# Performance work log

Hardware: AMD Instinct MI355X
Metric: run time of the kernel (lower is better)

Reference implementation:

```python
import jax, jax.numpy as jnp
import numpy as np

B, T, F, H, K = 64, 256, 16, 128, 3


def setup_inputs() -> dict:
    key = jax.random.key(0)
    ks = jax.random.split(key, 8)
    s = 1.0 / np.sqrt(H)
    x = jax.random.normal(ks[0], (B, T, F), jnp.float32)
    index = jnp.sort(jax.random.randint(ks[1], (B, 2), 0, T), axis=1)
    # per-feature LSTM params (input dim 1), torch gate order [i, f, g, o]
    W_ih = jax.random.uniform(ks[2], (F, 4 * H), jnp.float32, -s, s)
    W_hh = jax.random.uniform(ks[3], (F, 4 * H, H), jnp.float32, -s, s)
    b = jax.random.uniform(ks[4], (F, 4 * H), jnp.float32, -s, s)  # b_ih + b_hh folded
    conv_w = jax.random.uniform(ks[5], (K,), jnp.float32, -1.0 / np.sqrt(K), 1.0 / np.sqrt(K))
    fc_w = jax.random.uniform(ks[6], (F * H, 2), jnp.float32, -1.0 / np.sqrt(F * H), 1.0 / np.sqrt(F * H))
    fc_b = jax.random.uniform(ks[7], (2,), jnp.float32, -1.0 / np.sqrt(F * H), 1.0 / np.sqrt(F * H))
    return dict(x=x, index=index, W_ih=W_ih, W_hh=W_hh, b=b, conv_w=conv_w, fc_w=fc_w, fc_b=fc_b)


def reference(x, index, W_ih, W_hh, b, conv_w, fc_w, fc_b):
    Bn, Tn, Fn = x.shape
    Hn = W_hh.shape[-1]
    t = jnp.arange(Tn)
    # valid[b, t] = start <= t < end; recurrence only advances inside the ragged slice
    valid = (t[None, :] >= index[:, 0:1]) & (t[None, :] < index[:, 1:2])  # [B, T]
    xs = jnp.moveaxis(x, 1, 0)            # [T, B, F]
    ms = jnp.moveaxis(valid, 1, 0)[:, :, None, None]  # [T, B, 1, 1]

    def step(carry, inp):
        h, c = carry                       # [B, F, H] each
        x_t, m = inp                       # [B, F], [B, 1, 1]
        gates = x_t[:, :, None] * W_ih[None] \
            + jnp.einsum('bfh,fgh->bfg', h, W_hh) + b[None]  # [B, F, 4H]
        i, f, g, o = jnp.split(gates, 4, axis=-1)
        i = jax.nn.sigmoid(i); f = jax.nn.sigmoid(f)
        g = jnp.tanh(g); o = jax.nn.sigmoid(o)
        c_new = f * c + i * g
        h_new = o * jnp.tanh(c_new)
        h = jnp.where(m, h_new, h)
        c = jnp.where(m, c_new, c)
        return (h, c), None

    h0 = jnp.zeros((Bn, Fn, Hn), x.dtype)
    (h, _), _ = jax.lax.scan(step, (h0, h0), (xs, ms))
    outs = h                               # [B, F, H] == last LSTM output per slice

    cofs = outs.mean(axis=-1)              # AdaptiveAvgPool1d(1) -> [B, F]
    cofs = jax.lax.conv_general_dilated(
        cofs[:, None, :], conv_w[None, None, :], (1,), [(K // 2, K // 2)],
        dimension_numbers=('NCH', 'OIH', 'NCH'))[:, 0, :]  # [B, F]
    gate = jax.nn.sigmoid(cofs)
    outs = outs * gate[:, :, None]
    return outs.reshape(Bn, -1) @ fc_w + fc_b  # [B, 2]
```

## Files before the change

### kernel.cpp

```cpp
#include <hip/hip_runtime.h>

typedef _Float16 half_t;
typedef half_t half2_t __attribute__((ext_vector_type(2)));
typedef half_t half8  __attribute__((ext_vector_type(8)));
typedef unsigned int uint_t;
typedef uint_t uint4v __attribute__((ext_vector_type(4)));
typedef float float4v __attribute__((ext_vector_type(4)));

#define B_  64
#define T_  256
#define F_  16
#define H_  128
#define LOG2E 1.44269504f

__device__ __forceinline__ float rcp_(float x)  { return __builtin_amdgcn_rcpf(x); }
__device__ __forceinline__ float sigm2(float x) { return rcp_(1.0f + __builtin_amdgcn_exp2f(x * -LOG2E)); }
__device__ __forceinline__ float tanh2(float x) { return fmaf(rcp_(1.0f + __builtin_amdgcn_exp2f(x * (-2.0f * LOG2E))), 2.0f, -1.0f); }
__device__ __forceinline__ float sigm(float x)  { return rcp_(1.0f + __expf(-x)); }

__global__ void make_sched(const int* __restrict__ index, int* __restrict__ pairs) {
    __shared__ int ss[B_], ee[B_], mid[B_], bo[B_];
    const int t = threadIdx.x;
    const int s = index[2 * t], e = index[2 * t + 1];
    ss[t] = s; ee[t] = e; mid[t] = s + e;
    __syncthreads();
    int m = mid[t], r = 0;
    for (int j = 0; j < B_; ++j) r += (mid[j] < m) || (mid[j] == m && j < t);
    bo[r] = t;
    __syncthreads();
    if (t < 32) {
        int bA = bo[2 * t], bB = bo[2 * t + 1];
        int su = min(ss[bA], ss[bB]), eu = max(ee[bA], ee[bB]);
        int4 v;
        v.x = (bA << 8) | bB;
        v.y = (ss[bA] << 16) | ee[bA];
        v.z = (ss[bB] << 16) | ee[bB];
        v.w = (su << 16) | eu;
        ((int4*)pairs)[t] = v;
    }
}

__global__ void repack_w(const float* __restrict__ whh, uint_t* __restrict__ wt) {
    const int f = blockIdx.x, w = blockIdx.y, tid = threadIdx.x;
    const int lane = tid & 63, q4 = tid >> 6;
    const int li = lane & 15, lg = lane >> 4;
    const float* base = whh + (size_t)f * 512 * 128;
#pragma unroll
    for (int qq = 0; qq < 4; ++qq) {
        const int qf = q4 * 4 + qq;
        const int m = qf >> 2, kt = qf & 3;
        const int g512 = 128 * m + 16 * w + li;
        uint_t tmp[4];
#pragma unroll
        for (int e2 = 0; e2 < 4; ++e2) {
            int k = kt * 32 + lg * 8 + 2 * e2;
            half2_t h;
            h[0] = (half_t)base[g512 * 128 + k];
            h[1] = (half_t)base[g512 * 128 + k + 1];
            tmp[e2] = __builtin_bit_cast(uint_t, h);
        }
        uint4 out = { tmp[0], tmp[1], tmp[2], tmp[3] };
        ((uint4*)wt)[(((size_t)f * 8 + w) * 16 + qf) * 64 + lane] = out;
    }
}

__global__ __launch_bounds__(512, 4) void lstm_mfma(
    const float* __restrict__ x, const uint_t* __restrict__ wt,
    const float* __restrict__ wih_g, const float* __restrict__ bias_g,
    const int* __restrict__ pairs, float* __restrict__ hout)
{
    __shared__ float xsh[2][T_];
    __shared__ alignas(16) half_t hbuf[2][2][H_];

    const int f = blockIdx.x & 15;
    const int4 pv = ((const int4*)pairs)[blockIdx.x >> 4];
    const int bA = pv.x >> 8, bB = pv.x & 255;
    const int sA = pv.y >> 16, eA = pv.y & 0xffff;
    const int sB = pv.z >> 16, eB = pv.z & 0xffff;
    const int su = pv.w >> 16, eu = pv.w & 0xffff;

    const int tid = threadIdx.x, lane = tid & 63, w = tid >> 6;
    const int li = lane & 15, lg = lane >> 4;
    const int cell = 16 * w + li;
    const int hsel = li >> 3;
    const int csel = lg >> 1;

    uint4v wr[16];
    {
        const char* ws = (const char*)wt + ((((size_t)f * 8 + w) * 16) * 64 + lane) * 16;
#pragma unroll
        for (int q = 0; q < 16; ++q) {
            unsigned long long a = (unsigned long long)(ws + (size_t)q * 1024);
            asm volatile("global_load_dwordx4 %0, %1, off" : "=v"(wr[q]) : "v"(a));
        }
        asm volatile("s_waitcnt vmcnt(0)");
        __builtin_amdgcn_sched_barrier(0);
    }

    float wih[4], bb4[4];
#pragma unroll
    for (int m = 0; m < 4; ++m) {
        wih[m] = wih_g[f * 512 + 128 * m + cell];
        bb4[m] = bias_g[f * 512 + 128 * m + cell];
    }

    const int myb = csel ? bB : bA;
    const int mys = csel ? sB : sA;
    const int mye = csel ? eB : eA;

    {
        int bb_ = tid >> 8, tt = tid & 255;
        xsh[bb_][tt] = x[((size_t)(bb_ ? bB : bA) * T_ + tt) * F_ + f];
    }
    if (tid < 2 * H_) hbuf[0][tid >> 7][tid & 127] = (half_t)0.0f;

    float cst = 0.0f, hst = 0.0f;
    int pp = 0;
    __syncthreads();

    for (int t = su; t < eu; ++t) {
        const half_t* hb = &hbuf[pp][hsel][lg * 8];
        half8 a0 = *(const half8*)(hb + 0);
        half8 a1 = *(const half8*)(hb + 32);
        half8 a2 = *(const half8*)(hb + 64);
        half8 a3 = *(const half8*)(hb + 96);
        float xt = xsh[csel][t];

        float gv[4];
#pragma unroll
        for (int m = 0; m < 4; ++m) {
            float iv = fmaf(xt, wih[m], bb4[m]);
            float4v ca = { iv, iv, iv, iv };
            float4v cb = { 0.f, 0.f, 0.f, 0.f };
            ca = __builtin_amdgcn_mfma_f32_16x16x32_f16(a0, __builtin_bit_cast(half8, wr[m * 4 + 0]), ca, 0, 0, 0);
            cb = __builtin_amdgcn_mfma_f32_16x16x32_f16(a1, __builtin_bit_cast(half8, wr[m * 4 + 1]), cb, 0, 0, 0);
            ca = __builtin_amdgcn_mfma_f32_16x16x32_f16(a2, __builtin_bit_cast(half8, wr[m * 4 + 2]), ca, 0, 0, 0);
            cb = __builtin_amdgcn_mfma_f32_16x16x32_f16(a3, __builtin_bit_cast(half8, wr[m * 4 + 3]), cb, 0, 0, 0);
            gv[m] = ca[0] + cb[0];
        }

        float gi = sigm2(gv[0]);
        float gf = sigm2(gv[1]);
        float gg = tanh2(gv[2]);
        float go = sigm2(gv[3]);
        float cn = fmaf(gf, cst, gi * gg);
        bool mk = (t >= mys) & (t < mye);
        cst = mk ? cn : cst;
        float hn = go * tanh2(cst);
        hst = mk ? hn : hst;

        if (lg == 0)      hbuf[pp ^ 1][0][cell] = (half_t)hst;
        else if (lg == 2) hbuf[pp ^ 1][1][cell] = (half_t)hst;
        __syncthreads();
        pp ^= 1;
    }

    if ((lg & 1) == 0) hout[((size_t)myb * F_ + f) * H_ + cell] = hst;
}

__global__ void epilogue(const float* __restrict__ hout, const float* __restrict__ conv_w,
                         const float* __restrict__ fc_w, const float* __restrict__ fc_b,
                         float* __restrict__ out)
{
    const int b = blockIdx.x, t = threadIdx.x;
    const int lane = t & 63, wv = t >> 6;
    __shared__ float part[2][16];
    __shared__ float gate_sh[16];

    float hv[16];
#pragma unroll
    for (int f = 0; f < 16; ++f) hv[f] = hout[((size_t)b * 16 + f) * 128 + t];

#pragma unroll
    for (int f = 0; f < 16; ++f) {
        float s = hv[f];
#pragma unroll
        for (int off = 32; off >= 1; off >>= 1) s += __shfl_down(s, off, 64);
        if (lane == 0) part[wv][f] = s;
    }
    __syncthreads();
    if (t < 16) gate_sh[t] = (part[0][t] + part[1][t]) * (1.0f / 128.0f);
    __syncthreads();
    float gate = 0.0f;
    if (t < 16) {
        float l  = (t > 0)  ? gate_sh[t - 1] : 0.0f;
        float mi = gate_sh[t];
        float r  = (t < 15) ? gate_sh[t + 1] : 0.0f;
        gate = sigm(fmaf(l, conv_w[0], fmaf(mi, conv_w[1], r * conv_w[2])));
    }
    __syncthreads();
    if (t < 16) gate_sh[t] = gate;
    __syncthreads();

    float acc0 = 0.0f, acc1 = 0.0f;
    const float2* fw2 = (const float2*)fc_w;
#pragma unroll
    for (int f = 0; f < 16; ++f) {
        float hg = hv[f] * gate_sh[f];
        float2 w2 = fw2[f * 128 + t];
        acc0 = fmaf(hg, w2.x, acc0);
        acc1 = fmaf(hg, w2.y, acc1);
    }
#pragma unroll
    for (int off = 32; off >= 1; off >>= 1) {
        acc0 += __shfl_down(acc0, off, 64);
        acc1 += __shfl_down(acc1, off, 64);
    }
    if (lane == 0) { part[wv][0] = acc0; part[wv][1] = acc1; }
    __syncthreads();
    if (t == 0) {
        out[b * 2 + 0] = part[0][0] + part[1][0] + fc_b[0];
        out[b * 2 + 1] = part[0][1] + part[1][1] + fc_b[1];
    }
}

extern "C" void kernel_launch(void* const* d_in, const int* in_sizes, int n_in,
                              void* d_out, int out_size, void* d_ws, size_t ws_size,
                              hipStream_t stream) {
    const float* x      = (const float*)d_in[0];
    const int*   index  = (const int*)  d_in[1];
    const float* W_ih   = (const float*)d_in[2];
    const float* W_hh   = (const float*)d_in[3];
    const float* bias   = (const float*)d_in[4];
    const float* conv_w = (const float*)d_in[5];
    const float* fc_w   = (const float*)d_in[6];
    const float* fc_b   = (const float*)d_in[7];
    float* out = (float*)d_out;

    uint_t* wt    = (uint_t*)d_ws;
    float*  hout  = (float*)((char*)d_ws + 2 * 1024 * 1024);
    int*    pairs = (int*)((char*)d_ws + 2 * 1024 * 1024 + 512 * 1024);

    make_sched<<<1, 64, 0, stream>>>(index, pairs);
    repack_w<<<dim3(F_, 8), 256, 0, stream>>>(W_hh, wt);
    lstm_mfma<<<512, 512, 0, stream>>>(x, wt, W_ih, bias, pairs, hout);
    epilogue<<<B_, 128, 0, stream>>>(hout, conv_w, fc_w, fc_b, out);
}
```

Baseline: 146.5 us.

## Pack four batch sequences per LSTM block instead of two

Each LSTM block now processes four sorted batch elements per feature instead of two. The MFMA A operand's 16 rows now cover four distinct hidden vectors rather than two duplicated ones, so 256 blocks replace 512. This removes redundant MFMA work, and the blocks fit in a single wave on the device. The trade-off is that the union time range over four sequences is longer than over two, so some steps are wasted on masked entries. Padded shared-memory strides are added to reduce bank conflicts.

```diff
diff --git a/kernel.cpp b/kernel.cpp
--- a/kernel.cpp
+++ b/kernel.cpp
@@ -11,6 +11,8 @@
 #define T_  256
 #define F_  16
 #define H_  128
+#define HQ  144
+#define XQ  264
 #define LOG2E 1.44269504f
 
 __device__ __forceinline__ float rcp_(float x)  { return __builtin_amdgcn_rcpf(x); }
@@ -18,25 +20,23 @@
 __device__ __forceinline__ float tanh2(float x) { return fmaf(rcp_(1.0f + __builtin_amdgcn_exp2f(x * (-2.0f * LOG2E))), 2.0f, -1.0f); }
 __device__ __forceinline__ float sigm(float x)  { return rcp_(1.0f + __expf(-x)); }
 
-__global__ void make_sched(const int* __restrict__ index, int* __restrict__ pairs) {
-    __shared__ int ss[B_], ee[B_], mid[B_], bo[B_];
+__global__ void make_sched(const int* __restrict__ index, int* __restrict__ gmeta,
+                           int* __restrict__ guni) {
+    __shared__ int mid[B_], oB[B_], oS[B_], oE[B_];
     const int t = threadIdx.x;
     const int s = index[2 * t], e = index[2 * t + 1];
-    ss[t] = s; ee[t] = e; mid[t] = s + e;
+    mid[t] = s + e;
     __syncthreads();
     int m = mid[t], r = 0;
     for (int j = 0; j < B_; ++j) r += (mid[j] < m) || (mid[j] == m && j < t);
-    bo[r] = t;
-    __syncthreads();
-    if (t < 32) {
-        int bA = bo[2 * t], bB = bo[2 * t + 1];
-        int su = min(ss[bA], ss[bB]), eu = max(ee[bA], ee[bB]);
-        int4 v;
-        v.x = (bA << 8) | bB;
-        v.y = (ss[bA] << 16) | ee[bA];
-        v.z = (ss[bB] << 16) | ee[bB];
-        v.w = (su << 16) | eu;
-        ((int4*)pairs)[t] = v;
+    oB[r] = t; oS[r] = s; oE[r] = e;
+    __syncthreads();
+    int4 v; v.x = oB[t]; v.y = oS[t]; v.z = oE[t]; v.w = 0;
+    ((int4*)gmeta)[t] = v;
+    if (t < 16) {
+        int su = 1 << 30, eu = 0;
+        for (int j = 0; j < 4; ++j) { su = min(su, oS[4 * t + j]); eu = max(eu, oE[4 * t + j]); }
+        guni[2 * t] = su; guni[2 * t + 1] = eu;
     }
 }
 
@@ -67,76 +67,73 @@
 __global__ __launch_bounds__(512, 4) void lstm_mfma(
     const float* __restrict__ x, const uint_t* __restrict__ wt,
     const float* __restrict__ wih_g, const float* __restrict__ bias_g,
-    const int* __restrict__ pairs, float* __restrict__ hout)
+    const int* __restrict__ gmeta, const int* __restrict__ guni,
+    float* __restrict__ hout)
 {
-    __shared__ float xsh[2][T_];
-    __shared__ alignas(16) half_t hbuf[2][2][H_];
-
-    const int f = blockIdx.x & 15;
-    const int4 pv = ((const int4*)pairs)[blockIdx.x >> 4];
-    const int bA = pv.x >> 8, bB = pv.x & 255;
-    const int sA = pv.y >> 16, eA = pv.y & 0xffff;
-    const int sB = pv.z >> 16, eB = pv.z & 0xffff;
-    const int su = pv.w >> 16, eu = pv.w & 0xffff;
-
+    __shared__ float xsh[4][XQ];
+    __shared__ alignas(16) half_t hbuf[2][4][HQ];
+    __shared__ int bid4[4];
+
+    const int f = blockIdx.x & 15, q = blockIdx.x >> 4;
     const int tid = threadIdx.x, lane = tid & 63, w = tid >> 6;
     const int li = lane & 15, lg = lane >> 4;
+    const int ar = li >> 2;
     const int cell = 16 * w + li;
-    const int hsel = li >> 3;
-    const int csel = lg >> 1;
 
     uint4v wr[16];
     {
         const char* ws = (const char*)wt + ((((size_t)f * 8 + w) * 16) * 64 + lane) * 16;
 #pragma unroll
-        for (int q = 0; q < 16; ++q) {
-            unsigned long long a = (unsigned long long)(ws + (size_t)q * 1024);
-            asm volatile("global_load_dwordx4 %0, %1, off" : "=v"(wr[q]) : "v"(a));
+        for (int p = 0; p < 16; ++p) {
+            unsigned long long a = (unsigned long long)(ws + (size_t)p * 1024);
+            asm volatile("global_load_dwordx4 %0, %1, off" : "=v"(wr[p]) : "v"(a));
         }
         asm volatile("s_waitcnt vmcnt(0)");
         __builtin_amdgcn_sched_barrier(0);
     }
 
+    const int4 mymeta = ((const int4*)gmeta)[q * 4 + lg];
+    const int bmy = mymeta.x, mys = mymeta.y, mye = mymeta.z;
+    if (tid < 4) bid4[tid] = ((const int4*)gmeta)[q * 4 + tid].x;
+    const int su = guni[2 * q], eu = guni[2 * q + 1];
+
     float wih[4], bb4[4];
 #pragma unroll
     for (int m = 0; m < 4; ++m) {
         wih[m] = wih_g[f * 512 + 128 * m + cell];
         bb4[m] = bias_g[f * 512 + 128 * m + cell];
     }
-
-    const int myb = csel ? bB : bA;
-    const int mys = csel ? sB : sA;
-    const int mye = csel ? eB : eA;
-
-    {
-        int bb_ = tid >> 8, tt = tid & 255;
-        xsh[bb_][tt] = x[((size_t)(bb_ ? bB : bA) * T_ + tt) * F_ + f];
-    }
-    if (tid < 2 * H_) hbuf[0][tid >> 7][tid & 127] = (half_t)0.0f;
+    __syncthreads();
+
+#pragma unroll
+    for (int j = 0; j < 2; ++j) {
+        int idx = tid + 512 * j;
+        int c = idx >> 8, tt = idx & 255;
+        xsh[c][tt] = x[((size_t)bid4[c] * T_ + tt) * F_ + f];
+    }
+    hbuf[0][tid >> 7][tid & 127] = (half_t)0.0f;
 
     float cst = 0.0f, hst = 0.0f;
+    const float4v z4 = {0.f, 0.f, 0.f, 0.f};
     int pp = 0;
     __syncthreads();
 
     for (int t = su; t < eu; ++t) {
-        const half_t* hb = &hbuf[pp][hsel][lg * 8];
+        const half_t* hb = &hbuf[pp][ar][lg * 8];
         half8 a0 = *(const half8*)(hb + 0);
         half8 a1 = *(const half8*)(hb + 32);
         half8 a2 = *(const half8*)(hb + 64);
         half8 a3 = *(const half8*)(hb + 96);
-        float xt = xsh[csel][t];
+        float xt = xsh[lg][t];
 
         float gv[4];
 #pragma unroll
         for (int m = 0; m < 4; ++m) {
-            float iv = fmaf(xt, wih[m], bb4[m]);
-            float4v ca = { iv, iv, iv, iv };
-            float4v cb = { 0.f, 0.f, 0.f, 0.f };
-            ca = __builtin_amdgcn_mfma_f32_16x16x32_f16(a0, __builtin_bit_cast(half8, wr[m * 4 + 0]), ca, 0, 0, 0);
-            cb = __builtin_amdgcn_mfma_f32_16x16x32_f16(a1, __builtin_bit_cast(half8, wr[m * 4 + 1]), cb, 0, 0, 0);
+            float4v ca = __builtin_amdgcn_mfma_f32_16x16x32_f16(a0, __builtin_bit_cast(half8, wr[m * 4 + 0]), z4, 0, 0, 0);
+            float4v cb = __builtin_amdgcn_mfma_f32_16x16x32_f16(a1, __builtin_bit_cast(half8, wr[m * 4 + 1]), z4, 0, 0, 0);
             ca = __builtin_amdgcn_mfma_f32_16x16x32_f16(a2, __builtin_bit_cast(half8, wr[m * 4 + 2]), ca, 0, 0, 0);
             cb = __builtin_amdgcn_mfma_f32_16x16x32_f16(a3, __builtin_bit_cast(half8, wr[m * 4 + 3]), cb, 0, 0, 0);
-            gv[m] = ca[0] + cb[0];
+            gv[m] = (ca[0] + cb[0]) + fmaf(xt, wih[m], bb4[m]);
         }
 
         float gi = sigm2(gv[0]);
@@ -149,13 +146,12 @@
         float hn = go * tanh2(cst);
         hst = mk ? hn : hst;
 
-        if (lg == 0)      hbuf[pp ^ 1][0][cell] = (half_t)hst;
-        else if (lg == 2) hbuf[pp ^ 1][1][cell] = (half_t)hst;
+        hbuf[pp ^ 1][lg][cell] = (half_t)hst;
         __syncthreads();
         pp ^= 1;
     }
 
-    if ((lg & 1) == 0) hout[((size_t)myb * F_ + f) * H_ + cell] = hst;
+    hout[((size_t)bmy * F_ + f) * H_ + cell] = hst;
 }
 
 __global__ void epilogue(const float* __restrict__ hout, const float* __restrict__ conv_w,
@@ -229,10 +225,11 @@
 
     uint_t* wt    = (uint_t*)d_ws;
     float*  hout  = (float*)((char*)d_ws + 2 * 1024 * 1024);
-    int*    pairs = (int*)((char*)d_ws + 2 * 1024 * 1024 + 512 * 1024);
-
-    make_sched<<<1, 64, 0, stream>>>(index, pairs);
+    int*    gmeta = (int*)((char*)d_ws + 2 * 1024 * 1024 + 512 * 1024);
+    int*    guni  = (int*)((char*)d_ws + 2 * 1024 * 1024 + 512 * 1024 + 1024);
+
+    make_sched<<<1, 64, 0, stream>>>(index, gmeta, guni);
     repack_w<<<dim3(F_, 8), 256, 0, stream>>>(W_hh, wt);
-    lstm_mfma<<<512, 512, 0, stream>>>(x, wt, W_ih, bias, pairs, hout);
+    lstm_mfma<<<256, 512, 0, stream>>>(x, wt, W_ih, bias, gmeta, guni, hout);
     epilogue<<<B_, 128, 0, stream>>>(hout, conv_w, fc_w, fc_b, out);
 }
```

Result: faster. 122.5 us (-16.4%).
